# Kernel tuning notes

Hardware: AMD Instinct MI355X
Metric: run time of the kernel (lower is better)

Reference implementation:

```python
import jax, jax.numpy as jnp
import numpy as np

N = 100000      # nodes
E = 1600000     # edges (avg degree 16)
F_IN = 64       # input feature dim
H = 64          # hidden dim
R = 4           # relations
G = 512         # graphs in batch
C = 10          # classes
L = 3           # total conv layers (conv1 + L-1)
SCALE = 0.1


def setup_inputs() -> dict:
    key = jax.random.key(0)
    ks = jax.random.split(key, 12)
    x = jax.random.normal(ks[0], (N, F_IN), jnp.float32)
    edge_index = jax.random.randint(ks[1], (2, E), 0, N)
    edge_type = jax.random.randint(ks[2], (E,), 0, R)
    batch = jnp.sort(jax.random.randint(ks[3], (N,), 0, G))
    W1 = jax.random.normal(ks[4], (R, F_IN, H), jnp.float32) * SCALE
    root1 = jax.random.normal(ks[5], (F_IN, H), jnp.float32) * SCALE
    b1 = jnp.zeros((H,), jnp.float32)
    Wl = jax.random.normal(ks[6], (L - 1, R, H, H), jnp.float32) * SCALE
    rootl = jax.random.normal(ks[7], (L - 1, H, H), jnp.float32) * SCALE
    bl = jnp.zeros((L - 1, H), jnp.float32)
    lin1_w = jax.random.normal(ks[8], (H, H), jnp.float32) * SCALE
    lin1_b = jnp.zeros((H,), jnp.float32)
    lin2_w = jax.random.normal(ks[9], (H, C), jnp.float32) * SCALE
    lin2_b = jnp.zeros((C,), jnp.float32)
    return {"x": x, "edge_index": edge_index, "edge_type": edge_type,
            "batch": batch, "W1": W1, "root1": root1, "b1": b1,
            "Wl": Wl, "rootl": rootl, "bl": bl,
            "lin1_w": lin1_w, "lin1_b": lin1_b,
            "lin2_w": lin2_w, "lin2_b": lin2_b}


def _rgcn_conv(x, src, dst, edge_type, W, root, b):
    # Per-relation transform of all nodes (R small), then gather per edge.
    h = jnp.einsum('nd,rdf->rnf', x, W)          # [R, N, H]
    msg = h[edge_type, src]                      # [E, H] gather
    # Mean aggregation per (dst, relation): PyG RGCNConv default aggr='mean'.
    seg = dst * R + edge_type                    # combined (node, relation) id
    cnt = jax.ops.segment_sum(jnp.ones((msg.shape[0],), x.dtype), seg,
                              num_segments=x.shape[0] * R)
    norm = 1.0 / jnp.maximum(cnt[seg], 1.0)      # [E]
    agg = jax.ops.segment_sum(msg * norm[:, None], dst,
                              num_segments=x.shape[0])  # [N, H]
    return agg + x @ root + b


def _mean_pool(x, batch, num_graphs):
    s = jax.ops.segment_sum(x, batch, num_segments=num_graphs)
    cnt = jax.ops.segment_sum(jnp.ones((x.shape[0],), x.dtype), batch,
                              num_segments=num_graphs)
    return s / jnp.maximum(cnt, 1.0)[:, None]


def reference(x, edge_index, edge_type, batch, W1, root1, b1, Wl, rootl, bl,
              lin1_w, lin1_b, lin2_w, lin2_b):
    src, dst = edge_index[0], edge_index[1]
    h = jax.nn.relu(_rgcn_conv(x, src, dst, edge_type, W1, root1, b1))
    for i in range(L - 1):
        h = jax.nn.relu(_rgcn_conv(h, src, dst, edge_type, Wl[i], rootl[i], bl[i]))
    g = _mean_pool(h, batch, G)                  # [G, H]
    g = jax.nn.relu(g @ lin1_w + lin1_b)
    # dropout omitted (inference / training=False)
    return g @ lin2_w + lin2_b                   # [G, C]
```

## Files before the change

### kernel.cpp

```cpp
#include <hip/hip_runtime.h>

#define TILE 32
#define KDIM 320

typedef __attribute__((ext_vector_type(8))) short short8;
typedef __attribute__((ext_vector_type(4))) float f32x4;

__device__ inline unsigned short rne_bf16(float f) {
    union { float f; unsigned u; } x;
    x.f = f;
    unsigned r = (x.u + 0x7FFF + ((x.u >> 16) & 1)) >> 16;
    return (unsigned short)r;
}

__device__ inline float bf16_f(unsigned short v) {
    union { unsigned u; float f; } x;
    x.u = ((unsigned)v) << 16;
    return x.f;
}


__global__ void k_count(const int* __restrict__ dst, const int* __restrict__ typ,
                        int* __restrict__ cnt4, int* __restrict__ rank, int E) {
    int e = blockIdx.x * 256 + threadIdx.x;
    if (e < E) {
        int seg = dst[e] * 4 + typ[e];
        rank[e] = atomicAdd(&cnt4[seg], 1);
    }
}

__global__ void k_scan1(const int* __restrict__ in, int* __restrict__ out,
                        int* __restrict__ bsum, int M) {
    __shared__ int s[256];
    int t = threadIdx.x;
    int base = blockIdx.x * 1024 + t * 4;
    int v0 = (base + 0 < M) ? in[base + 0] : 0;
    int v1 = (base + 1 < M) ? in[base + 1] : 0;
    int v2 = (base + 2 < M) ? in[base + 2] : 0;
    int v3 = (base + 3 < M) ? in[base + 3] : 0;
    int ts = v0 + v1 + v2 + v3;
    s[t] = ts;
    __syncthreads();
    for (int off = 1; off < 256; off <<= 1) {
        int x = (t >= off) ? s[t - off] : 0;
        __syncthreads();
        s[t] += x;
        __syncthreads();
    }
    int excl = (t == 0) ? 0 : s[t - 1];
    if (t == 255) bsum[blockIdx.x] = s[255];
    if (base + 0 < M) out[base + 0] = excl;
    if (base + 1 < M) out[base + 1] = excl + v0;
    if (base + 2 < M) out[base + 2] = excl + v0 + v1;
    if (base + 3 < M) out[base + 3] = excl + v0 + v1 + v2;
}

__global__ void k_scan2(const int* __restrict__ bsum, int* __restrict__ boff, int nb) {
    __shared__ int s[512];
    int t = threadIdx.x;
    s[t] = (t < nb) ? bsum[t] : 0;
    __syncthreads();
    for (int off = 1; off < 512; off <<= 1) {
        int x = (t >= off) ? s[t - off] : 0;
        __syncthreads();
        s[t] += x;
        __syncthreads();
    }
    if (t < nb) boff[t] = (t == 0) ? 0 : s[t - 1];
}

__global__ void k_scan3(int* __restrict__ out, const int* __restrict__ boff, int M, int E) {
    int i = blockIdx.x * 256 + threadIdx.x;
    if (i < M) out[i] += boff[i >> 10];
    else if (i == M) out[M] = E;
}

__global__ void k_fill(const int* __restrict__ src, const int* __restrict__ dst,
                       const int* __restrict__ typ, const int* __restrict__ start4,
                       const int* __restrict__ rank, int* __restrict__ elist, int E) {
    int e = blockIdx.x * 256 + threadIdx.x;
    if (e < E) {
        int seg = dst[e] * 4 + typ[e];
        elist[start4[seg] + rank[e]] = src[e];
    }
}


__global__ void k_prep(const float* __restrict__ x, unsigned short* __restrict__ xb, int ncvt,
                       const float* __restrict__ W1, const float* __restrict__ root1,
                       const float* __restrict__ Wl, const float* __restrict__ rootl,
                       unsigned short* __restrict__ Wp, int nwp,
                       const int* __restrict__ batch, int* __restrict__ gstart,
                       int nN, int nG) {
    int b = blockIdx.x;
    if (b < ncvt) {
        int i = (b * 256 + threadIdx.x) * 4;
        float4 v = *reinterpret_cast<const float4*>(&x[i]);
        ushort4 o;
        o.x = rne_bf16(v.x); o.y = rne_bf16(v.y);
        o.z = rne_bf16(v.z); o.w = rne_bf16(v.w);
        *reinterpret_cast<ushort4*>(&xb[i]) = o;
        return;
    }
    b -= ncvt;
    if (b < nwp) {
        int idx = b * 256 + threadIdx.x;
        const int TOT = 3 * 320 * 64;
        if (idx >= TOT) return;
        int j = idx & 7;
        int lane = (idx >> 3) & 63;
        int t = idx >> 9;
        int ks = t % 10;
        int lnt = t / 10;
        int nt = lnt & 3;
        int layer = lnt >> 2;
        int k = ks * 32 + ((lane >> 4) << 3) + j;
        int h = nt * 16 + (lane & 15);
        float v;
        if (k < 256) {
            v = (layer == 0) ? W1[k * 64 + h] : Wl[(layer - 1) * 16384 + k * 64 + h];
        } else {
            v = (layer == 0) ? root1[(k - 256) * 64 + h]
                             : rootl[(layer - 1) * 4096 + (k - 256) * 64 + h];
        }
        Wp[idx] = rne_bf16(v);
        return;
    }
    b -= nwp;
    {
        int n = b * 256 + threadIdx.x;
        if (n >= nN) return;
        int bb = batch[n];
        if (n == 0) {
            for (int g = 0; g <= bb; ++g) gstart[g] = 0;
        } else {
            int bp = batch[n - 1];
            for (int g = bp + 1; g <= bb; ++g) gstart[g] = n;
        }
        if (n == nN - 1) {
            for (int g = bb + 1; g <= nG; ++g) gstart[g] = nN;
        }
    }
}


__global__ __launch_bounds__(256, 6) void k_conv(
        const unsigned short* __restrict__ hin, unsigned short* __restrict__ hout,
        const int* __restrict__ elist, const int* __restrict__ start4,
        const unsigned short* __restrict__ Wp, const float* __restrict__ bias, int nN) {
    __shared__ unsigned short A2[TILE * KDIM];
    const int tid = threadIdx.x;
    const int lane = tid & 63;
    const int wvs = __builtin_amdgcn_readfirstlane(tid >> 6);
    const int wv = tid >> 6;
    const int tile = blockIdx.x * TILE;

    for (int jj = 0; jj < 8; ++jj) {
        const int nl = wvs * 8 + jj;
        const int n = tile + nl;
        unsigned short* Arow = &A2[nl * KDIM];
        const int sw = (((lane >> 3) ^ (nl & 7)) << 3) + (lane & 7);
        if (n >= nN) {
#pragma unroll
            for (int seg = 0; seg < 5; ++seg) Arow[seg * 64 + sw] = 0;
            continue;
        }
        const int e0 = __builtin_amdgcn_readfirstlane(start4[n * 4 + 0]);
        const int e1 = __builtin_amdgcn_readfirstlane(start4[n * 4 + 1]);
        const int e2 = __builtin_amdgcn_readfirstlane(start4[n * 4 + 2]);
        const int e3 = __builtin_amdgcn_readfirstlane(start4[n * 4 + 3]);
        const int e4 = __builtin_amdgcn_readfirstlane(start4[n * 4 + 4]);

        unsigned short selfb = hin[((size_t)n << 6) + lane];
        float S0 = 0.f, S1 = 0.f, S2 = 0.f, S3 = 0.f;
        int p = e0;

        for (; p + 8 <= e4; p += 8) {
            int qidx[8];
#pragma unroll
            for (int u = 0; u < 8; ++u)
                qidx[u] = __builtin_amdgcn_readfirstlane(elist[p + u]);
            unsigned short vb[8];
#pragma unroll
            for (int u = 0; u < 8; ++u)
                vb[u] = hin[((size_t)qidx[u] << 6) + lane];
            __builtin_amdgcn_sched_barrier(0);
#pragma unroll
            for (int u = 0; u < 8; ++u) {
                float t = bf16_f(vb[u]);
                int q = p + u;
                S0 += t;
                S1 += (q >= e1) ? t : 0.f;
                S2 += (q >= e2) ? t : 0.f;
                S3 += (q >= e3) ? t : 0.f;
            }
        }
        if (p < e4) {
            int qidx[8];
#pragma unroll
            for (int u = 0; u < 8; ++u) {
                int q = p + u;
                int qc = (q < e4) ? q : (e4 - 1);
                qidx[u] = __builtin_amdgcn_readfirstlane(elist[qc]);
            }
            unsigned short vb[8];
#pragma unroll
            for (int u = 0; u < 8; ++u)
                vb[u] = hin[((size_t)qidx[u] << 6) + lane];
            __builtin_amdgcn_sched_barrier(0);
#pragma unroll
            for (int u = 0; u < 8; ++u) {
                int q = p + u;
                float t = (q < e4) ? bf16_f(vb[u]) : 0.f;
                S0 += t;
                S1 += (q >= e1) ? t : 0.f;
                S2 += (q >= e2) ? t : 0.f;
                S3 += (q >= e3) ? t : 0.f;
            }
        }

        int c0 = e1 - e0, c1 = e2 - e1, c2 = e3 - e2, c3 = e4 - e3;
        float a0 = (S0 - S1) * ((c0 > 0) ? 1.0f / (float)c0 : 0.f);
        float a1 = (S1 - S2) * ((c1 > 0) ? 1.0f / (float)c1 : 0.f);
        float a2 = (S2 - S3) * ((c2 > 0) ? 1.0f / (float)c2 : 0.f);
        float a3 = S3 * ((c3 > 0) ? 1.0f / (float)c3 : 0.f);
        Arow[0   + sw] = rne_bf16(a0);
        Arow[64  + sw] = rne_bf16(a1);
        Arow[128 + sw] = rne_bf16(a2);
        Arow[192 + sw] = rne_bf16(a3);
        Arow[256 + sw] = selfb;
    }
    __syncthreads();

    const int mt = wv & 1;
    const int ntb = (wv >> 1) << 1;
    const int nloc = mt * 16 + (lane & 15);
    f32x4 acc0 = {0.f, 0.f, 0.f, 0.f};
    f32x4 acc1 = {0.f, 0.f, 0.f, 0.f};
    const unsigned short* wp0 = Wp + ((size_t)(ntb * 10) * 64 + lane) * 8;
    const unsigned short* wp1 = Wp + ((size_t)((ntb + 1) * 10) * 64 + lane) * 8;
#pragma unroll 2
    for (int ks = 0; ks < 10; ++ks) {
        int kc = ks * 4 + (lane >> 4);
        int swz = (kc & ~7) | ((kc & 7) ^ (lane & 7));
        short8 a = *reinterpret_cast<const short8*>(&A2[nloc * KDIM + swz * 8]);
        short8 b0 = *reinterpret_cast<const short8*>(&wp0[ks * 512]);
        short8 b1 = *reinterpret_cast<const short8*>(&wp1[ks * 512]);
        acc0 = __builtin_amdgcn_mfma_f32_16x16x32_bf16(a, b0, acc0, 0, 0, 0);
        acc1 = __builtin_amdgcn_mfma_f32_16x16x32_bf16(a, b1, acc1, 0, 0, 0);
    }
    const int h0 = ntb * 16 + (lane & 15);
    const int nr = tile + mt * 16 + ((lane >> 4) << 2);
    const float bb0 = bias[h0];
    const float bb1 = bias[h0 + 16];
#pragma unroll
    for (int r = 0; r < 4; ++r) {
        int n = nr + r;
        if (n < nN) {
            hout[(size_t)n * 64 + h0]      = rne_bf16(fmaxf(acc0[r] + bb0, 0.f));
            hout[(size_t)n * 64 + h0 + 16] = rne_bf16(fmaxf(acc1[r] + bb1, 0.f));
        }
    }
}


__global__ void k_poolmlp(const unsigned short* __restrict__ h,
                          const int* __restrict__ gstart,
                          const float* __restrict__ w1, const float* __restrict__ b1,
                          const float* __restrict__ w2, const float* __restrict__ b2,
                          float* __restrict__ out) {
    __shared__ float red[4][64];
    __shared__ float sg[64];
    __shared__ float sh[64];
    int g = blockIdx.x;
    int t = threadIdx.x;
    int f = t & 63;
    int sl = t >> 6;
    int s = gstart[g], e = gstart[g + 1];
    float acc = 0.f;
    for (int n = s + sl; n < e; n += 4)
        acc += bf16_f(h[(size_t)n * 64 + f]);
    red[sl][f] = acc;
    __syncthreads();
    if (sl == 0) {
        int c = e - s;
        float m = (red[0][f] + red[1][f] + red[2][f] + red[3][f]) /
                  (float)((c > 0) ? c : 1);
        sg[f] = m;
    }
    __syncthreads();
    if (sl == 0) {
        float a = b1[f];
#pragma unroll 16
        for (int k = 0; k < 64; ++k) a += sg[k] * w1[k * 64 + f];
        sh[f] = fmaxf(a, 0.f);
    }
    __syncthreads();
    if (t < 10) {
        float o = b2[t];
#pragma unroll 16
        for (int k = 0; k < 64; ++k) o += sh[k] * w2[k * 10 + t];
        out[g * 10 + t] = o;
    }
}


extern "C" void kernel_launch(void* const* d_in, const int* in_sizes, int n_in,
                              void* d_out, int out_size, void* d_ws, size_t ws_size,
                              hipStream_t stream) {
    const float* x     = (const float*)d_in[0];
    const int*   ei    = (const int*)d_in[1];
    const int*   et    = (const int*)d_in[2];
    const int*   batch = (const int*)d_in[3];
    const float* W1    = (const float*)d_in[4];
    const float* root1 = (const float*)d_in[5];
    const float* b1    = (const float*)d_in[6];
    const float* Wl    = (const float*)d_in[7];
    const float* rootl = (const float*)d_in[8];
    const float* bl    = (const float*)d_in[9];
    const float* l1w   = (const float*)d_in[10];
    const float* l1b   = (const float*)d_in[11];
    const float* l2w   = (const float*)d_in[12];
    const float* l2b   = (const float*)d_in[13];
    float* out = (float*)d_out;

    const int N = in_sizes[3];
    const int E = in_sizes[2];
    const int G = out_size / 10;
    const int M = 4 * N;

    const int* src = ei;
    const int* dst = ei + E;

    char* base = (char*)d_ws;
    size_t off = 0;
    auto carve = [&](size_t bytes) {
        char* p = base + off;
        off = (off + bytes + 511) & ~(size_t)511;
        return p;
    };
    int*   cnt4    = (int*)carve((size_t)M * 4);
    int*   start4  = (int*)carve((size_t)(M + 1) * 4);
    int*   rank    = (int*)carve((size_t)E * 4);
    int*   elist   = (int*)carve((size_t)E * 4);
    int*   bsum    = (int*)carve(512 * 4);
    int*   boff    = (int*)carve(512 * 4);
    unsigned short* Wpack = (unsigned short*)carve((size_t)3 * 320 * 64 * 2);
    unsigned short* xb    = (unsigned short*)carve((size_t)N * 64 * 2);
    unsigned short* hb_a  = (unsigned short*)carve((size_t)N * 64 * 2);
    unsigned short* hb_b  = (unsigned short*)carve((size_t)N * 64 * 2);
    int*   gstart  = (int*)carve((size_t)(G + 1) * 4);
    (void)ws_size;

    hipMemsetAsync(cnt4, 0, (size_t)M * 4, stream);

    k_count<<<(E + 255) / 256, 256, 0, stream>>>(dst, et, cnt4, rank, E);

    int nb = (M + 1023) / 1024;
    k_scan1<<<nb, 256, 0, stream>>>(cnt4, start4, bsum, M);
    k_scan2<<<1, 512, 0, stream>>>(bsum, boff, nb);
    k_scan3<<<(M + 1 + 255) / 256, 256, 0, stream>>>(start4, boff, M, E);
    k_fill<<<(E + 255) / 256, 256, 0, stream>>>(src, dst, et, start4, rank, elist, E);

    const int ncvt = (N * 64 / 4 + 255) / 256;
    const int nwp  = (3 * 320 * 64 + 255) / 256;
    const int ngb  = (N + 255) / 256;
    k_prep<<<ncvt + nwp + ngb, 256, 0, stream>>>(x, xb, ncvt, W1, root1, Wl, rootl,
                                                 Wpack, nwp, batch, gstart, N, G);

    const int cb = (N + TILE - 1) / TILE;
    const int WSTRIDE = 320 * 64;
    k_conv<<<cb, 256, 0, stream>>>(xb,   hb_a, elist, start4, Wpack,               b1,      N);
    k_conv<<<cb, 256, 0, stream>>>(hb_a, hb_b, elist, start4, Wpack + WSTRIDE,     bl,      N);
    k_conv<<<cb, 256, 0, stream>>>(hb_b, hb_a, elist, start4, Wpack + 2 * WSTRIDE, bl + 64, N);

    k_poolmlp<<<G, 256, 0, stream>>>(hb_a, gstart, l1w, l1b, l2w, l2b, out);
}
```

Baseline: 344.5 us.

## Fuse edge counting into prep kernel and widen gather unroll in conv

Merges the edge-count/rank atomic kernel into the prep kernel launch, removing one launch. In the conv kernel, each wave preloads its 33 CSR start offsets into scalar registers up front, and the neighbor gather is unrolled from 8 to 32 edges per iteration. Relation masking now uses scalar 0/1 FMAs instead of selects, and the launch-bounds occupancy hint goes from 6 to 8. The wider unroll puts more loads in flight but raises register pressure and wastes more work on the padded tail, since average degree is about 16.

Result: slower. 507.3 us (+47.3%).

```diff
diff --git a/kernel.cpp b/kernel.cpp
--- a/kernel.cpp
+++ b/kernel.cpp
@@ -19,15 +19,8 @@
     return x.f;
 }
 
-
-__global__ void k_count(const int* __restrict__ dst, const int* __restrict__ typ,
-                        int* __restrict__ cnt4, int* __restrict__ rank, int E) {
-    int e = blockIdx.x * 256 + threadIdx.x;
-    if (e < E) {
-        int seg = dst[e] * 4 + typ[e];
-        rank[e] = atomicAdd(&cnt4[seg], 1);
-    }
-}
+#define SMASK(cond) __int_as_float(__builtin_amdgcn_readfirstlane((cond) ? 0x3f800000 : 0))
+
 
 __global__ void k_scan1(const int* __restrict__ in, int* __restrict__ out,
                         int* __restrict__ bsum, int M) {
@@ -86,13 +79,24 @@
 }
 
 
-__global__ void k_prep(const float* __restrict__ x, unsigned short* __restrict__ xb, int ncvt,
+__global__ void k_prep(const int* __restrict__ dst, const int* __restrict__ typ,
+                       int* __restrict__ cnt4, int* __restrict__ rank, int E, int necnt,
+                       const float* __restrict__ x, unsigned short* __restrict__ xb, int ncvt,
                        const float* __restrict__ W1, const float* __restrict__ root1,
                        const float* __restrict__ Wl, const float* __restrict__ rootl,
                        unsigned short* __restrict__ Wp, int nwp,
                        const int* __restrict__ batch, int* __restrict__ gstart,
                        int nN, int nG) {
     int b = blockIdx.x;
+    if (b < necnt) {
+        int e = b * 256 + threadIdx.x;
+        if (e < E) {
+            int seg = dst[e] * 4 + typ[e];
+            rank[e] = atomicAdd(&cnt4[seg], 1);
+        }
+        return;
+    }
+    b -= necnt;
     if (b < ncvt) {
         int i = (b * 256 + threadIdx.x) * 4;
         float4 v = *reinterpret_cast<const float4*>(&x[i]);
@@ -144,7 +148,7 @@
 }
 
 
-__global__ __launch_bounds__(256, 6) void k_conv(
+__global__ __launch_bounds__(256, 8) void k_conv(
         const unsigned short* __restrict__ hin, unsigned short* __restrict__ hout,
         const int* __restrict__ elist, const int* __restrict__ start4,
         const unsigned short* __restrict__ Wp, const float* __restrict__ bias, int nN) {
@@ -155,6 +159,16 @@
     const int wv = tid >> 6;
     const int tile = blockIdx.x * TILE;
 
+    const int sbase = (tile + wvs * 8) * 4;
+    const int smax = nN * 4;
+    int s4[33];
+#pragma unroll
+    for (int i = 0; i < 33; ++i) {
+        int idx = sbase + i;
+        s4[i] = __builtin_amdgcn_readfirstlane(start4[(idx < smax) ? idx : smax]);
+    }
+
+#pragma unroll
     for (int jj = 0; jj < 8; ++jj) {
         const int nl = wvs * 8 + jj;
         const int n = tile + nl;
@@ -165,57 +179,57 @@
             for (int seg = 0; seg < 5; ++seg) Arow[seg * 64 + sw] = 0;
             continue;
         }
-        const int e0 = __builtin_amdgcn_readfirstlane(start4[n * 4 + 0]);
-        const int e1 = __builtin_amdgcn_readfirstlane(start4[n * 4 + 1]);
-        const int e2 = __builtin_amdgcn_readfirstlane(start4[n * 4 + 2]);
-        const int e3 = __builtin_amdgcn_readfirstlane(start4[n * 4 + 3]);
-        const int e4 = __builtin_amdgcn_readfirstlane(start4[n * 4 + 4]);
+        const int e0 = s4[jj * 4 + 0];
+        const int e1 = s4[jj * 4 + 1];
+        const int e2 = s4[jj * 4 + 2];
+        const int e3 = s4[jj * 4 + 3];
+        const int e4 = s4[jj * 4 + 4];
 
         unsigned short selfb = hin[((size_t)n << 6) + lane];
         float S0 = 0.f, S1 = 0.f, S2 = 0.f, S3 = 0.f;
         int p = e0;
 
-        for (; p + 8 <= e4; p += 8) {
-            int qidx[8];
-#pragma unroll
-            for (int u = 0; u < 8; ++u)
-                qidx[u] = __builtin_amdgcn_readfirstlane(elist[p + u]);
-            unsigned short vb[8];
-#pragma unroll
-            for (int u = 0; u < 8; ++u)
-                vb[u] = hin[((size_t)qidx[u] << 6) + lane];
+        for (; p + 32 <= e4; p += 32) {
+            int q[32];
+#pragma unroll
+            for (int u = 0; u < 32; ++u)
+                q[u] = __builtin_amdgcn_readfirstlane(elist[p + u]);
+            unsigned short vb[32];
+#pragma unroll
+            for (int u = 0; u < 32; ++u)
+                vb[u] = hin[((size_t)q[u] << 6) + lane];
             __builtin_amdgcn_sched_barrier(0);
 #pragma unroll
-            for (int u = 0; u < 8; ++u) {
+            for (int u = 0; u < 32; ++u) {
                 float t = bf16_f(vb[u]);
-                int q = p + u;
+                int qq = p + u;
                 S0 += t;
-                S1 += (q >= e1) ? t : 0.f;
-                S2 += (q >= e2) ? t : 0.f;
-                S3 += (q >= e3) ? t : 0.f;
+                S1 = fmaf(t, SMASK(qq >= e1), S1);
+                S2 = fmaf(t, SMASK(qq >= e2), S2);
+                S3 = fmaf(t, SMASK(qq >= e3), S3);
             }
         }
         if (p < e4) {
-            int qidx[8];
-#pragma unroll
-            for (int u = 0; u < 8; ++u) {
-                int q = p + u;
-                int qc = (q < e4) ? q : (e4 - 1);
-                qidx[u] = __builtin_amdgcn_readfirstlane(elist[qc]);
+            int q[32];
+#pragma unroll
+            for (int u = 0; u < 32; ++u) {
+                int qq = p + u;
+                int qc = (qq < e4) ? qq : (e4 - 1);
+                q[u] = __builtin_amdgcn_readfirstlane(elist[qc]);
             }
-            unsigned short vb[8];
-#pragma unroll
-            for (int u = 0; u < 8; ++u)
-                vb[u] = hin[((size_t)qidx[u] << 6) + lane];
+            unsigned short vb[32];
+#pragma unroll
+            for (int u = 0; u < 32; ++u)
+                vb[u] = hin[((size_t)q[u] << 6) + lane];
             __builtin_amdgcn_sched_barrier(0);
 #pragma unroll
-            for (int u = 0; u < 8; ++u) {
-                int q = p + u;
-                float t = (q < e4) ? bf16_f(vb[u]) : 0.f;
+            for (int u = 0; u < 32; ++u) {
+                int qq = p + u;
+                float t = bf16_f(vb[u]) * SMASK(qq < e4);
                 S0 += t;
-                S1 += (q >= e1) ? t : 0.f;
-                S2 += (q >= e2) ? t : 0.f;
-                S3 += (q >= e3) ? t : 0.f;
+                S1 = fmaf(t, SMASK(qq >= e1), S1);
+                S2 = fmaf(t, SMASK(qq >= e2), S2);
+                S3 = fmaf(t, SMASK(qq >= e3), S3);
             }
         }
 
@@ -354,7 +368,14 @@
 
     hipMemsetAsync(cnt4, 0, (size_t)M * 4, stream);
 
-    k_count<<<(E + 255) / 256, 256, 0, stream>>>(dst, et, cnt4, rank, E);
+    const int necnt = (E + 255) / 256;
+    const int ncvt = (N * 64 / 4 + 255) / 256;
+    const int nwp  = (3 * 320 * 64 + 255) / 256;
+    const int ngb  = (N + 255) / 256;
+    k_prep<<<necnt + ncvt + nwp + ngb, 256, 0, stream>>>(
+        dst, et, cnt4, rank, E, necnt,
+        x, xb, ncvt, W1, root1, Wl, rootl, Wpack, nwp,
+        batch, gstart, N, G);
 
     int nb = (M + 1023) / 1024;
     k_scan1<<<nb, 256, 0, stream>>>(cnt4, start4, bsum, M);
@@ -362,12 +383,6 @@
     k_scan3<<<(M + 1 + 255) / 256, 256, 0, stream>>>(start4, boff, M, E);
     k_fill<<<(E + 255) / 256, 256, 0, stream>>>(src, dst, et, start4, rank, elist, E);
 
-    const int ncvt = (N * 64 / 4 + 255) / 256;
-    const int nwp  = (3 * 320 * 64 + 255) / 256;
-    const int ngb  = (N + 255) / 256;
-    k_prep<<<ncvt + nwp + ngb, 256, 0, stream>>>(x, xb, ncvt, W1, root1, Wl, rootl,
-                                                 Wpack, nwp, batch, gstart, N, G);
-
     const int cb = (N + TILE - 1) / TILE;
     const int WSTRIDE = 320 * 64;
     k_conv<<<cb, 256, 0, stream>>>(xb,   hb_a, elist, start4, Wpack,               b1,      N);
```
